# Kernel tuning notes

Hardware: AMD Instinct MI355X
Metric: run time of the kernel (lower is better)

The kernel has to match this reference:

```python
import jax, jax.numpy as jnp
import numpy as np

INPUT_SIZE = 32   # activity vocab
HIDDEN = 512
OUT = 33          # OUT-1 activity logits + 1 duration
COND = 128
LAYERS = 2
MAXLEN = 64
BATCH = 256
SOS = 0
SLOPE = 0.01      # LeakyReLU default negative slope

def _leaky(x):
    return jnp.where(x >= 0, x, SLOPE * x)

def setup_inputs() -> dict:
    key = jax.random.key(0)
    ks = jax.random.split(key, 16)
    s = 0.05  # small init scale keeps gates in a sane range
    return {
        "batch_size": BATCH,
        "h0": jax.random.normal(ks[0], (LAYERS, BATCH, HIDDEN), jnp.float32),
        "c0": jax.random.normal(ks[1], (LAYERS, BATCH, HIDDEN), jnp.float32),
        "conditionals": jax.random.normal(ks[2], (BATCH, COND), jnp.float32),
        "emb": jax.random.normal(ks[3], (INPUT_SIZE, HIDDEN - 1), jnp.float32) * s,
        "Wih": jax.random.normal(ks[4], (LAYERS, 4 * HIDDEN, HIDDEN), jnp.float32) * s,
        "Whh": jax.random.normal(ks[5], (LAYERS, 4 * HIDDEN, HIDDEN), jnp.float32) * s,
        "bih": jax.random.normal(ks[6], (LAYERS, 4 * HIDDEN), jnp.float32) * s,
        "bhh": jax.random.normal(ks[7], (LAYERS, 4 * HIDDEN), jnp.float32) * s,
        "fcW": jax.random.normal(ks[8], (HIDDEN, COND), jnp.float32) * s,
        "fcb": jax.random.normal(ks[9], (HIDDEN,), jnp.float32) * s,
        "fc2W": jax.random.normal(ks[10], (HIDDEN, HIDDEN), jnp.float32) * s,
        "fc2b": jax.random.normal(ks[11], (HIDDEN,), jnp.float32) * s,
        "fc3W": jax.random.normal(ks[12], (OUT, HIDDEN), jnp.float32) * s,
        "fc3b": jax.random.normal(ks[13], (OUT,), jnp.float32) * s,
    }

def reference(batch_size, h0, c0, conditionals, emb, Wih, Whh, bih, bhh,
              fcW, fcb, fc2W, fc2b, fc3W, fc3b):
    B = h0.shape[1]
    # conditionals branch is step-invariant: compute once (same math as per-step fc+LeakyReLU)
    cond = _leaky(conditionals @ fcW.T + fcb)  # [B, H]
    # decoder_input = zeros[B,1,2] with act channel = sos
    inp0 = jnp.concatenate(
        [jnp.full((B, 1), float(SOS), jnp.float32), jnp.zeros((B, 1), jnp.float32)], axis=-1)

    def step(carry, _):
        h, c, inp = carry  # h,c: [L,B,H], inp: [B,2]
        # CustomDurationEmbedding: embed act index, concat duration channel -> [B,H]
        x = jnp.concatenate([emb[inp[:, 0].astype(jnp.int32)], inp[:, 1:]], axis=-1)
        hs, cs = [], []
        for l in range(LAYERS):  # seq_len==1 per step -> one LSTM cell per layer
            g = x @ Wih[l].T + bih[l] + h[l] @ Whh[l].T + bhh[l]  # [B,4H]
            i_g, f_g, g_g, o_g = jnp.split(g, 4, axis=-1)         # torch gate order i,f,g,o
            c_l = jax.nn.sigmoid(f_g) * c[l] + jax.nn.sigmoid(i_g) * jnp.tanh(g_g)
            h_l = jax.nn.sigmoid(o_g) * jnp.tanh(c_l)
            hs.append(h_l); cs.append(c_l)
            x = h_l
        h_new, c_new = jnp.stack(hs), jnp.stack(cs)
        # conditional_add: (lstm_out + cond) -> fc2 -> LeakyReLU -> fc3
        pred = _leaky((x + cond) @ fc2W.T + fc2b) @ fc3W.T + fc3b  # [B,OUT]
        # pack: topk(1) over activity logits; softmax over singleton seq dim == 1.0
        act = jnp.argmax(pred[:, :OUT - 1], axis=-1).astype(pred.dtype)[:, None]
        dur = jnp.ones((B, 1), pred.dtype)
        nxt = jnp.concatenate([act, dur], axis=-1)
        return (h_new, c_new, nxt), pred

    _, outs = jax.lax.scan(step, (h0, c0, inp0), None, length=MAXLEN)  # [T,B,OUT]
    outs = jnp.transpose(outs, (1, 0, 2))  # [B,T,OUT]
    acts_log_probs = jax.nn.log_softmax(outs[..., :OUT - 1], axis=-1)
    durations = jax.nn.softmax(outs[..., OUT - 1:], axis=1)  # Softmax(dim=-2): over time
    return jnp.concatenate([acts_log_probs, durations], axis=-1)
```

## Files before the change

### kernel.cpp

```cpp
#include <hip/hip_runtime.h>
#include <math.h>

#define BB   256
#define HH   512
#define NWG  256
#define NTHR 1024
#define TT   64
#define NOUT 33
#define CD   128
#define SZ   (HH*BB)
#define LOFF (4*HH*HH)
#define BOFF (4*HH)
#define WBLK (16*1024)

typedef float f16v __attribute__((ext_vector_type(16)));
typedef float f8v  __attribute__((ext_vector_type(8)));
typedef const __attribute__((address_space(4))) float  cfloat;
typedef const __attribute__((address_space(4))) f16v   cf16v;
typedef const __attribute__((address_space(4))) f8v    cf8v;

__device__ __forceinline__ float sigm(float x)  { return 1.0f/(1.0f+expf(-x)); }
__device__ __forceinline__ float lrelu(float x) { return x >= 0.0f ? x : 0.01f*x; }

__device__ __forceinline__ float gld(const float* p) {
  return __hip_atomic_load(p, __ATOMIC_RELAXED, __HIP_MEMORY_SCOPE_AGENT);
}
__device__ __forceinline__ void gst(float* p, float v) {
  __hip_atomic_store(p, v, __ATOMIC_RELAXED, __HIP_MEMORY_SCOPE_AGENT);
}

__device__ __forceinline__ cfloat* cptr(const float* p) {
  unsigned long long u = (unsigned long long)p;
  unsigned lo = __builtin_amdgcn_readfirstlane((unsigned)u);
  unsigned hi = __builtin_amdgcn_readfirstlane((unsigned)(u >> 32));
  return (cfloat*)((((unsigned long long)hi) << 32) | (unsigned long long)lo);
}

__device__ __forceinline__ void gbar(unsigned* bar, unsigned ep, int grp, bool fence) {
  __syncthreads();
  if (threadIdx.x == 0) {
    if (fence) __builtin_amdgcn_fence(__ATOMIC_RELEASE, "agent");
    unsigned old = __hip_atomic_fetch_add(&bar[grp*16], 1u, __ATOMIC_RELAXED, __HIP_MEMORY_SCOPE_AGENT);
    if (old == ep*32u + 31u) {
      unsigned o2 = __hip_atomic_fetch_add(&bar[128], 1u, __ATOMIC_RELAXED, __HIP_MEMORY_SCOPE_AGENT);
      if (o2 == ep*8u + 7u)
        __hip_atomic_store(&bar[144], ep+1u, __ATOMIC_RELAXED, __HIP_MEMORY_SCOPE_AGENT);
    }
    while (__hip_atomic_load(&bar[144], __ATOMIC_RELAXED, __HIP_MEMORY_SCOPE_AGENT) < ep+1u)
      __builtin_amdgcn_s_sleep(1);
    if (fence) __builtin_amdgcn_fence(__ATOMIC_ACQUIRE, "agent");
  }
  __syncthreads();
}

extern "C" __global__ void __launch_bounds__(256)
transpose_weights(const float* __restrict__ Wih, const float* __restrict__ Whh,
                  float* __restrict__ wsT)
{
  const int w   = blockIdx.x;
  const int tid = threadIdx.x;
  float* dst = wsT + w*WBLK;
  #pragma unroll 1
  for (int j = 0; j < 64; ++j) {
    int i  = j*256 + tid;
    int ri = i >> 10, k = i & 1023;
    int l  = k >> 9,  kk = k & 511;
    int r2 = ri & 7,  u = r2 >> 2, g = r2 & 3;
    const float* src = (ri < 8) ? Wih : Whh;
    dst[k*16 + ri] = src[l*LOFF + (g*HH + 2*w + u)*HH + kk];
  }
}

__device__ __forceinline__ void FMA2(const f16v& w, float x0, float x1,
                                     float h0, float h1, float* acc) {
  #pragma unroll
  for (int r = 0; r < 8; ++r) {
    acc[r*2+0] += w[r]*x0;
    acc[r*2+1] += w[r]*x1;
  }
  #pragma unroll
  for (int r = 0; r < 8; ++r) {
    acc[r*2+0] += w[8+r]*h0;
    acc[r*2+1] += w[8+r]*h1;
  }
}

__device__ __forceinline__ void lstm_phase(const float* __restrict__ wT,
    const float* __restrict__ bias, float* __restrict__ red,
    const float* __restrict__ xsrc, const float* __restrict__ hsrc,
    float* __restrict__ hdst, float* __restrict__ cbuf,
    int hu0, int tid, int ks, int bg)
{
  const int lane  = tid & 63;
  const int kbase = ks*64;
  const int b0    = bg*128 + lane;
  cf16v* wk = (cf16v*)cptr(wT + kbase*16);
  const float* xp = xsrc + kbase*BB + b0;
  const float* hp = hsrc + kbase*BB + b0;

  float acc[16];
  #pragma unroll
  for (int r = 0; r < 16; ++r) acc[r] = 0.0f;

  float qx[4], qh[4], px[4], ph[4];
  #pragma unroll
  for (int j = 0; j < 2; ++j) {
    qx[j*2] = gld(xp + j*BB); qx[j*2+1] = gld(xp + j*BB + 64);
    qh[j*2] = gld(hp + j*BB); qh[j*2+1] = gld(hp + j*BB + 64);
  }
  #pragma unroll 1
  for (int it = 0; it < 32; ++it) {
    f16v w0 = wk[it*2+0];
    f16v w1 = wk[it*2+1];
    if (it+1 < 32) {
      #pragma unroll
      for (int j = 0; j < 2; ++j) {
        px[j*2]   = gld(xp + (it*2+2+j)*BB);  px[j*2+1] = gld(xp + (it*2+2+j)*BB + 64);
        ph[j*2]   = gld(hp + (it*2+2+j)*BB);  ph[j*2+1] = gld(hp + (it*2+2+j)*BB + 64);
      }
    }
    FMA2(w0, qx[0], qx[1], qh[0], qh[1], acc);
    FMA2(w1, qx[2], qx[3], qh[2], qh[3], acc);
    #pragma unroll
    for (int j = 0; j < 4; ++j) { qx[j] = px[j]; qh[j] = ph[j]; }
  }
  #pragma unroll
  for (int r = 0; r < 8; ++r) {
    red[(ks*8 + r)*BB + b0]      = acc[r*2];
    red[(ks*8 + r)*BB + b0 + 64] = acc[r*2+1];
  }
  __syncthreads();
  if (tid < 512) {
    const int b = tid & 255, u = tid >> 8;
    float g[4];
    #pragma unroll
    for (int gg = 0; gg < 4; ++gg) {
      float s = bias[u*4+gg];
      #pragma unroll
      for (int k2 = 0; k2 < 8; ++k2) s += red[(k2*8 + u*4+gg)*BB + b];
      g[gg] = s;
    }
    const int hu = hu0 + u;
    float ig = sigm(g[0]), fg = sigm(g[1]);
    float gv = tanhf(g[2]), og = sigm(g[3]);
    float cn = fg*cbuf[hu*BB+b] + ig*gv;
    cbuf[hu*BB+b] = cn;
    gst(hdst + hu*BB + b, og*tanhf(cn));
  }
}

extern "C" __global__ void __launch_bounds__(NTHR)
decoder_kernel(const float* __restrict__ h0, const float* __restrict__ c0,
               const float* __restrict__ conds, const float* __restrict__ emb,
               const float* __restrict__ wsT, const float* __restrict__ bih,
               const float* __restrict__ bhh, const float* __restrict__ fcW,
               const float* __restrict__ fcb, const float* __restrict__ fc2W,
               const float* __restrict__ fc2b, const float* __restrict__ fc3W,
               const float* __restrict__ fc3b,
               float* __restrict__ out, unsigned* bar, float* wsf)
{
  const int w   = blockIdx.x;
  const int tid = threadIdx.x;
  const int hu0 = 2*w;
  const int grp = w & 7;
  const int wv  = tid >> 6;
  const int bg  = wv & 1;
  const int ks  = wv >> 1;

  float* xbuf  = wsf;
  float* h1b0  = wsf + 1*SZ;
  float* h1b1  = wsf + 2*SZ;
  float* h2b0  = wsf + 3*SZ;
  float* h2b1  = wsf + 4*SZ;
  float* c1b   = wsf + 5*SZ;
  float* c2b   = wsf + 6*SZ;
  float* condb = wsf + 7*SZ;
  float* yb    = wsf + 8*SZ;
  float* condY = wsf + 9*SZ;

  const float* wT1 = wsT + w*WBLK;
  const float* wT2 = wsT + w*WBLK + 512*16;

  __shared__ float red[64*BB];
  __shared__ float bias1[8], bias2[8], biasc[2];
  __shared__ float lds_y[HH];
  __shared__ float part[NOUT][17];
  __shared__ int   lds_act;
  __shared__ float lds_pad[4096];
  if (tid == 0) ((volatile float*)lds_pad)[0] = 0.0f;

  if (tid < 512) {
    const int b = tid & 255, u = tid >> 8;
    const int k = hu0 + u;
    xbuf[k*BB+b] = (k < HH-1) ? emb[k] : 0.0f;
    h1b0[k*BB+b] = h0[b*HH + k];
    c1b [k*BB+b] = c0[b*HH + k];
    h2b0[k*BB+b] = h0[(BB+b)*HH + k];
    c2b [k*BB+b] = c0[(BB+b)*HH + k];
    float a = fcb[k];
    const float4* cp = (const float4*)(conds + b*CD);
    const float4* wp = (const float4*)(fcW + k*CD);
    #pragma unroll 8
    for (int q = 0; q < CD/4; ++q) {
      float4 c4 = cp[q], w4 = wp[q];
      a += c4.x*w4.x + c4.y*w4.y + c4.z*w4.z + c4.w*w4.w;
    }
    condb[k*BB+b] = lrelu(a);
  }
  if (tid < 8) {
    int u = tid >> 2, g = tid & 3;
    bias1[tid] = bih[g*HH + hu0 + u] + bhh[g*HH + hu0 + u];
    bias2[tid] = bih[BOFF + g*HH + hu0 + u] + bhh[BOFF + g*HH + hu0 + u];
  }
  if (tid < 2) biasc[tid] = fc2b[hu0 + tid];

  unsigned ep = 0;
  gbar(bar, ep++, grp, true);

  if (tid < 512) {
    const int b = tid & 255, u = tid >> 8;
    cfloat* wr = cptr(fc2W + (hu0+u)*HH);
    float s = 0.0f;
    #pragma unroll 4
    for (int k = 0; k < HH; k += 4) {
      s += wr[k]*condb[k*BB+b]     + wr[k+1]*condb[(k+1)*BB+b]
         + wr[k+2]*condb[(k+2)*BB+b] + wr[k+3]*condb[(k+3)*BB+b];
    }
    condY[(hu0+u)*BB + b] = s;
  }
  __syncthreads();

  for (int t = 0; t < TT; ++t) {
    const bool par = (t & 1) != 0;
    float* h1r = par ? h1b1 : h1b0;
    float* h1w = par ? h1b0 : h1b1;
    float* h2r = par ? h2b1 : h2b0;
    float* h2w = par ? h2b0 : h2b1;

    lstm_phase(wT1, bias1, red, xbuf, h1r, h1w, c1b, hu0, tid, ks, bg);
    gbar(bar, ep++, grp, false);
    lstm_phase(wT2, bias2, red, h1w, h2r, h2w, c2b, hu0, tid, ks, bg);
    gbar(bar, ep++, grp, false);
    {
      const int b = tid & 255, s4 = tid >> 8;
      const float* hp = h2w + (s4*128)*BB + b;
      cf8v* w0v = (cf8v*)cptr(fc2W + (hu0+0)*HH + s4*128);
      cf8v* w1v = (cf8v*)cptr(fc2W + (hu0+1)*HH + s4*128);
      float a0 = 0.0f, a1 = 0.0f;
      float q[8], pq[8];
      #pragma unroll
      for (int j = 0; j < 8; ++j) q[j] = gld(hp + j*BB);
      #pragma unroll 1
      for (int it = 0; it < 16; ++it) {
        f8v wa = w0v[it];
        f8v wb = w1v[it];
        if (it+1 < 16) {
          #pragma unroll
          for (int j = 0; j < 8; ++j) pq[j] = gld(hp + (it*8+8+j)*BB);
        }
        #pragma unroll
        for (int j = 0; j < 8; ++j) { a0 += wa[j]*q[j]; a1 += wb[j]*q[j]; }
        #pragma unroll
        for (int j = 0; j < 8; ++j) q[j] = pq[j];
      }
      red[(s4*2+0)*BB + b] = a0;
      red[(s4*2+1)*BB + b] = a1;
    }
    __syncthreads();
    if (tid < 512) {
      const int b = tid & 255, u = tid >> 8;
      float s = biasc[u] + condY[(hu0+u)*BB + b];
      #pragma unroll
      for (int s4 = 0; s4 < 4; ++s4) s += red[(s4*2+u)*BB + b];
      gst(yb + (hu0+u)*BB + b, lrelu(s));
    }
    gbar(bar, ep++, grp, false);
    {
      if (tid < 512) lds_y[tid] = gld(yb + tid*BB + w);
      __syncthreads();
      int o = 0, kc = 0;
      bool active = false;
      if (tid < 512)        { o = tid & 31; kc = tid >> 5; active = true; }
      else if (tid < 528)   { o = 32;       kc = tid - 512; active = true; }
      if (active) {
        float p = 0.0f;
        const float* fw = fc3W + o*HH + kc*32;
        #pragma unroll
        for (int k2 = 0; k2 < 32; ++k2) p += fw[k2] * lds_y[kc*32 + k2];
        part[o][kc] = p;
      }
      __syncthreads();
      float predv = -1e30f;
      if (tid < NOUT) {
        float s = fc3b[tid];
        #pragma unroll
        for (int kc2 = 0; kc2 < 16; ++kc2) s += part[tid][kc2];
        predv = s;
        out[(w*TT + t)*NOUT + tid] = s;
      }
      if (tid < 64) {
        float v  = (tid < 32) ? predv : -1e30f;
        int  idx = tid;
        #pragma unroll
        for (int off = 32; off > 0; off >>= 1) {
          float ov = __shfl_xor(v, off);
          int   oi = __shfl_xor(idx, off);
          if (ov > v || (ov == v && oi < idx)) { v = ov; idx = oi; }
        }
        if (tid == 0) lds_act = idx;
      }
      __syncthreads();
      const int act = lds_act;
      if (tid < 512)
        gst(xbuf + tid*BB + w, (tid < 511) ? emb[act*(HH-1) + tid] : 1.0f);
    }
    gbar(bar, ep++, grp, false);
  }

  if (tid < TT) {
    const int s = tid;
    float* po = out + (w*TT + s)*NOUT;
    float v[NOUT];
    #pragma unroll
    for (int o = 0; o < NOUT; ++o) v[o] = po[o];
    float m = v[0];
    #pragma unroll
    for (int o = 1; o < 32; ++o) m = fmaxf(m, v[o]);
    float sum = 0.0f;
    #pragma unroll
    for (int o = 0; o < 32; ++o) sum += expf(v[o] - m);
    float lse = m + logf(sum);
    #pragma unroll
    for (int o = 0; o < 32; ++o) po[o] = v[o] - lse;
    float d = v[32];
    float dm = d;
    #pragma unroll
    for (int off = 32; off > 0; off >>= 1) dm = fmaxf(dm, __shfl_xor(dm, off));
    float e = expf(d - dm);
    float es = e;
    #pragma unroll
    for (int off = 32; off > 0; off >>= 1) es += __shfl_xor(es, off);
    po[32] = e / es;
  }
}

extern "C" void kernel_launch(void* const* d_in, const int* in_sizes, int n_in,
                              void* d_out, int out_size, void* d_ws, size_t ws_size,
                              hipStream_t stream) {
  const float* h0   = (const float*)d_in[1];
  const float* c0   = (const float*)d_in[2];
  const float* cnd  = (const float*)d_in[3];
  const float* emb  = (const float*)d_in[4];
  const float* Wih  = (const float*)d_in[5];
  const float* Whh  = (const float*)d_in[6];
  const float* bih  = (const float*)d_in[7];
  const float* bhh  = (const float*)d_in[8];
  const float* fcW  = (const float*)d_in[9];
  const float* fcb  = (const float*)d_in[10];
  const float* fc2W = (const float*)d_in[11];
  const float* fc2b = (const float*)d_in[12];
  const float* fc3W = (const float*)d_in[13];
  const float* fc3b = (const float*)d_in[14];

  unsigned* bar = (unsigned*)d_ws;
  float* wsf = (float*)((char*)d_ws + 1024);
  float* wsT = wsf + 10*SZ;

  (void)hipMemsetAsync(d_ws, 0, 1024, stream);

  hipLaunchKernelGGL(transpose_weights, dim3(NWG), dim3(256), 0, stream,
                     Wih, Whh, wsT);
  hipLaunchKernelGGL(decoder_kernel, dim3(NWG), dim3(NTHR), 0, stream,
                     h0, c0, cnd, emb, wsT, bih, bhh, fcW, fcb,
                     fc2W, fc2b, fc3W, fc3b, (float*)d_out, bar, wsf);
}
```

Baseline: 3.731 ms.

## Repartition LSTM work into 4-unit by 128-batch tiles with register cell state

Each workgroup now owns 4 hidden units for half the batch instead of 2 units for the full batch. This halves the per-workgroup weight footprint re-read from the scalar cache relative to the activations and keeps the cell state in registers instead of a global buffer. The fc2 matvec uses a pre-transposed weight block and vectorized float2 activation loads with deeper prefetch. The cost is that each block re-reads the full activation vectors for its half-batch, and the transposed weight layout and barrier schedule change.

```diff
diff --git a/kernel.cpp b/kernel.cpp
--- a/kernel.cpp
+++ b/kernel.cpp
@@ -3,21 +3,18 @@
 
 #define BB   256
 #define HH   512
-#define NWG  256
-#define NTHR 1024
 #define TT   64
 #define NOUT 33
 #define CD   128
+#define NTHR 1024
+#define NWG  256
+#define LOFF (4*HH*HH)
 #define SZ   (HH*BB)
-#define LOFF (4*HH*HH)
-#define BOFF (4*HH)
-#define WBLK (16*1024)
+#define FC2OFF 4194304
 
 typedef float f16v __attribute__((ext_vector_type(16)));
-typedef float f8v  __attribute__((ext_vector_type(8)));
-typedef const __attribute__((address_space(4))) float  cfloat;
-typedef const __attribute__((address_space(4))) f16v   cf16v;
-typedef const __attribute__((address_space(4))) f8v    cf8v;
+typedef const __attribute__((address_space(4))) float cfloat;
+typedef const __attribute__((address_space(4))) f16v  cf16v;
 
 __device__ __forceinline__ float sigm(float x)  { return 1.0f/(1.0f+expf(-x)); }
 __device__ __forceinline__ float lrelu(float x) { return x >= 0.0f ? x : 0.01f*x; }
@@ -25,8 +22,16 @@
 __device__ __forceinline__ float gld(const float* p) {
   return __hip_atomic_load(p, __ATOMIC_RELAXED, __HIP_MEMORY_SCOPE_AGENT);
 }
+__device__ __forceinline__ float2 gld2(const float* p) {
+  unsigned long long v = __hip_atomic_load((const unsigned long long*)p,
+                                           __ATOMIC_RELAXED, __HIP_MEMORY_SCOPE_AGENT);
+  union { unsigned long long u; float2 f; } c; c.u = v; return c.f;
+}
 __device__ __forceinline__ void gst(float* p, float v) {
   __hip_atomic_store(p, v, __ATOMIC_RELAXED, __HIP_MEMORY_SCOPE_AGENT);
+}
+__device__ __forceinline__ unsigned gldu(const unsigned* p) {
+  return __hip_atomic_load(p, __ATOMIC_RELAXED, __HIP_MEMORY_SCOPE_AGENT);
 }
 
 __device__ __forceinline__ cfloat* cptr(const float* p) {
@@ -46,8 +51,7 @@
       if (o2 == ep*8u + 7u)
         __hip_atomic_store(&bar[144], ep+1u, __ATOMIC_RELAXED, __HIP_MEMORY_SCOPE_AGENT);
     }
-    while (__hip_atomic_load(&bar[144], __ATOMIC_RELAXED, __HIP_MEMORY_SCOPE_AGENT) < ep+1u)
-      __builtin_amdgcn_s_sleep(1);
+    while (gldu(&bar[144]) < ep+1u) __builtin_amdgcn_s_sleep(1);
     if (fence) __builtin_amdgcn_fence(__ATOMIC_ACQUIRE, "agent");
   }
   __syncthreads();
@@ -55,236 +59,234 @@
 
 extern "C" __global__ void __launch_bounds__(256)
 transpose_weights(const float* __restrict__ Wih, const float* __restrict__ Whh,
-                  float* __restrict__ wsT)
+                  const float* __restrict__ fc2W, float* __restrict__ wsT)
 {
-  const int w   = blockIdx.x;
-  const int tid = threadIdx.x;
-  float* dst = wsT + w*WBLK;
+  const int i = blockIdx.x, tid = threadIdx.x;
+  float* dst = wsT + (size_t)i*32768;
   #pragma unroll 1
-  for (int j = 0; j < 64; ++j) {
-    int i  = j*256 + tid;
-    int ri = i >> 10, k = i & 1023;
-    int l  = k >> 9,  kk = k & 511;
-    int r2 = ri & 7,  u = r2 >> 2, g = r2 & 3;
-    const float* src = (ri < 8) ? Wih : Whh;
-    dst[k*16 + ri] = src[l*LOFF + (g*HH + 2*w + u)*HH + kk];
-  }
-}
-
-__device__ __forceinline__ void FMA2(const f16v& w, float x0, float x1,
-                                     float h0, float h1, float* acc) {
-  #pragma unroll
-  for (int r = 0; r < 8; ++r) {
-    acc[r*2+0] += w[r]*x0;
-    acc[r*2+1] += w[r]*x1;
-  }
-  #pragma unroll
-  for (int r = 0; r < 8; ++r) {
-    acc[r*2+0] += w[8+r]*h0;
-    acc[r*2+1] += w[8+r]*h1;
-  }
-}
-
-__device__ __forceinline__ void lstm_phase(const float* __restrict__ wT,
+  for (int idx = tid; idx < 32768; idx += 256) {
+    int slot = idx & 15, k = (idx>>4)&511, rh = (idx>>13)&1, l = (idx>>14)&1;
+    int a = slot>>3, r = slot&7, u = r>>2, g = r&3;
+    int hu = i*4 + rh*2 + u;
+    const float* src = a ? Whh : Wih;
+    dst[idx] = src[(size_t)l*LOFF + (size_t)(g*HH+hu)*HH + k];
+  }
+  float* dstf = wsT + FC2OFF + (size_t)i*2048;
+  #pragma unroll 1
+  for (int idx = tid; idx < 2048; idx += 256) {
+    int r = idx & 3, k = idx >> 2;
+    dstf[idx] = fc2W[(size_t)(i*4+r)*HH + k];
+  }
+}
+
+__device__ __forceinline__ void lstm_phase(const float* __restrict__ wTl,
     const float* __restrict__ bias, float* __restrict__ red,
     const float* __restrict__ xsrc, const float* __restrict__ hsrc,
-    float* __restrict__ hdst, float* __restrict__ cbuf,
-    int hu0, int tid, int ks, int bg)
+    float* __restrict__ hdst, float& creg, int i, int j, int tid)
 {
-  const int lane  = tid & 63;
-  const int kbase = ks*64;
-  const int b0    = bg*128 + lane;
-  cf16v* wk = (cf16v*)cptr(wT + kbase*16);
-  const float* xp = xsrc + kbase*BB + b0;
-  const float* hp = hsrc + kbase*BB + b0;
+  const int lane = tid & 63, wvid = tid >> 6;
+  const int rh = wvid & 1, ks = wvid >> 1;
+  cf16v* wp = (cf16v*)cptr(wTl + ((size_t)rh*512 + ks*64)*16);
+  const int bo = j*128 + 2*lane;
+  const float* xp = xsrc + (size_t)(ks*64)*BB + bo;
+  const float* hp = hsrc + (size_t)(ks*64)*BB + bo;
 
   float acc[16];
   #pragma unroll
-  for (int r = 0; r < 16; ++r) acc[r] = 0.0f;
-
-  float qx[4], qh[4], px[4], ph[4];
-  #pragma unroll
-  for (int j = 0; j < 2; ++j) {
-    qx[j*2] = gld(xp + j*BB); qx[j*2+1] = gld(xp + j*BB + 64);
-    qh[j*2] = gld(hp + j*BB); qh[j*2+1] = gld(hp + j*BB + 64);
-  }
+  for (int r = 0; r < 16; ++r) acc[r] = 0.f;
+
+  float2 qx[2], qh[2], px[2], ph[2], rx[2], rhb[2];
+  #pragma unroll
+  for (int kk = 0; kk < 2; ++kk) { qx[kk]=gld2(xp+kk*BB);     qh[kk]=gld2(hp+kk*BB); }
+  #pragma unroll
+  for (int kk = 0; kk < 2; ++kk) { px[kk]=gld2(xp+(2+kk)*BB); ph[kk]=gld2(hp+(2+kk)*BB); }
+
   #pragma unroll 1
-  for (int it = 0; it < 32; ++it) {
-    f16v w0 = wk[it*2+0];
-    f16v w1 = wk[it*2+1];
-    if (it+1 < 32) {
-      #pragma unroll
-      for (int j = 0; j < 2; ++j) {
-        px[j*2]   = gld(xp + (it*2+2+j)*BB);  px[j*2+1] = gld(xp + (it*2+2+j)*BB + 64);
-        ph[j*2]   = gld(hp + (it*2+2+j)*BB);  ph[j*2+1] = gld(hp + (it*2+2+j)*BB + 64);
-      }
-    }
-    FMA2(w0, qx[0], qx[1], qh[0], qh[1], acc);
-    FMA2(w1, qx[2], qx[3], qh[2], qh[3], acc);
-    #pragma unroll
-    for (int j = 0; j < 4; ++j) { qx[j] = px[j]; qh[j] = ph[j]; }
-  }
-  #pragma unroll
-  for (int r = 0; r < 8; ++r) {
-    red[(ks*8 + r)*BB + b0]      = acc[r*2];
-    red[(ks*8 + r)*BB + b0 + 64] = acc[r*2+1];
-  }
+  for (int g = 0; g < 32; ++g) {
+    if (g+2 < 32) {
+      #pragma unroll
+      for (int kk = 0; kk < 2; ++kk) {
+        rx[kk]  = gld2(xp + (g*2+4+kk)*BB);
+        rhb[kk] = gld2(hp + (g*2+4+kk)*BB);
+      }
+    }
+    #pragma unroll
+    for (int kk = 0; kk < 2; ++kk) {
+      f16v w = wp[g*2+kk];
+      float2 xv = qx[kk], hv = qh[kk];
+      #pragma unroll
+      for (int r = 0; r < 8; ++r) {
+        acc[r*2+0] += w[r]*xv.x + w[8+r]*hv.x;
+        acc[r*2+1] += w[r]*xv.y + w[8+r]*hv.y;
+      }
+    }
+    #pragma unroll
+    for (int kk = 0; kk < 2; ++kk) {
+      qx[kk]=px[kk]; qh[kk]=ph[kk]; px[kk]=rx[kk]; ph[kk]=rhb[kk];
+    }
+  }
+  #pragma unroll
+  for (int r = 0; r < 8; ++r)
+    *(float2*)(red + (size_t)(ks*16 + rh*8 + r)*128 + 2*lane) = make_float2(acc[r*2], acc[r*2+1]);
   __syncthreads();
   if (tid < 512) {
-    const int b = tid & 255, u = tid >> 8;
-    float g[4];
+    const int lhu = tid >> 7, b = tid & 127;
+    float g4[4];
     #pragma unroll
     for (int gg = 0; gg < 4; ++gg) {
-      float s = bias[u*4+gg];
-      #pragma unroll
-      for (int k2 = 0; k2 < 8; ++k2) s += red[(k2*8 + u*4+gg)*BB + b];
-      g[gg] = s;
-    }
-    const int hu = hu0 + u;
-    float ig = sigm(g[0]), fg = sigm(g[1]);
-    float gv = tanhf(g[2]), og = sigm(g[3]);
-    float cn = fg*cbuf[hu*BB+b] + ig*gv;
-    cbuf[hu*BB+b] = cn;
-    gst(hdst + hu*BB + b, og*tanhf(cn));
+      float s = bias[lhu*4+gg];
+      #pragma unroll
+      for (int q = 0; q < 8; ++q) s += red[(q*16 + lhu*4+gg)*128 + b];
+      g4[gg] = s;
+    }
+    float ig=sigm(g4[0]), fg=sigm(g4[1]), gv=tanhf(g4[2]), og=sigm(g4[3]);
+    float cn = fg*creg + ig*gv;
+    creg = cn;
+    gst(hdst + (size_t)(i*4+lhu)*BB + j*128 + b, og*tanhf(cn));
+  }
+}
+
+__device__ __forceinline__ void fc2_phase(const float* __restrict__ h2src,
+    const float* __restrict__ wsTf, float* __restrict__ yb,
+    const float* lds_bc, const float* condY_l, float* __restrict__ red,
+    int i, int j, int tid)
+{
+  const int lane = tid & 63, ks2 = tid >> 6;
+  cf16v* wp = (cf16v*)cptr(wsTf + (size_t)ks2*128);
+  const int bo = j*128 + 2*lane;
+  const float* hp = h2src + (size_t)(ks2*32)*BB + bo;
+  float acc[8];
+  #pragma unroll
+  for (int r = 0; r < 8; ++r) acc[r] = 0.f;
+  float2 qh[4], ph[4];
+  #pragma unroll
+  for (int kk = 0; kk < 4; ++kk) qh[kk] = gld2(hp + kk*BB);
+  #pragma unroll 1
+  for (int g = 0; g < 8; ++g) {
+    if (g+1 < 8) {
+      #pragma unroll
+      for (int kk = 0; kk < 4; ++kk) ph[kk] = gld2(hp + (g*4+4+kk)*BB);
+    }
+    f16v w = wp[g];
+    #pragma unroll
+    for (int kk = 0; kk < 4; ++kk) {
+      float2 hv = qh[kk];
+      #pragma unroll
+      for (int r = 0; r < 4; ++r) {
+        acc[r*2+0] += w[kk*4+r]*hv.x;
+        acc[r*2+1] += w[kk*4+r]*hv.y;
+      }
+    }
+    #pragma unroll
+    for (int kk = 0; kk < 4; ++kk) qh[kk] = ph[kk];
+  }
+  #pragma unroll
+  for (int r = 0; r < 4; ++r)
+    *(float2*)(red + (size_t)(ks2*4+r)*128 + 2*lane) = make_float2(acc[r*2], acc[r*2+1]);
+  __syncthreads();
+  if (tid < 512) {
+    int r = tid >> 7, b = tid & 127;
+    float s = lds_bc[r] + condY_l[r*128+b];
+    #pragma unroll
+    for (int q = 0; q < 16; ++q) s += red[(q*4+r)*128 + b];
+    gst(yb + (size_t)(i*4+r)*BB + j*128 + b, lrelu(s));
   }
 }
 
 extern "C" __global__ void __launch_bounds__(NTHR)
 decoder_kernel(const float* __restrict__ h0, const float* __restrict__ c0,
                const float* __restrict__ conds, const float* __restrict__ emb,
-               const float* __restrict__ wsT, const float* __restrict__ bih,
+               const float* __restrict__ wsTW, const float* __restrict__ bih,
                const float* __restrict__ bhh, const float* __restrict__ fcW,
                const float* __restrict__ fcb, const float* __restrict__ fc2W,
                const float* __restrict__ fc2b, const float* __restrict__ fc3W,
                const float* __restrict__ fc3b,
                float* __restrict__ out, unsigned* bar, float* wsf)
 {
-  const int w   = blockIdx.x;
+  const int w = blockIdx.x;
+  const int i = w & 127, j = w >> 7;
+  const int grp = w & 7;
   const int tid = threadIdx.x;
-  const int hu0 = 2*w;
-  const int grp = w & 7;
-  const int wv  = tid >> 6;
-  const int bg  = wv & 1;
-  const int ks  = wv >> 1;
 
   float* xbuf  = wsf;
-  float* h1b0  = wsf + 1*SZ;
-  float* h1b1  = wsf + 2*SZ;
-  float* h2b0  = wsf + 3*SZ;
-  float* h2b1  = wsf + 4*SZ;
-  float* c1b   = wsf + 5*SZ;
-  float* c2b   = wsf + 6*SZ;
-  float* condb = wsf + 7*SZ;
-  float* yb    = wsf + 8*SZ;
-  float* condY = wsf + 9*SZ;
-
-  const float* wT1 = wsT + w*WBLK;
-  const float* wT2 = wsT + w*WBLK + 512*16;
-
-  __shared__ float red[64*BB];
-  __shared__ float bias1[8], bias2[8], biasc[2];
+  float* h1a = wsf + 1*SZ;  float* h1b = wsf + 2*SZ;
+  float* h2a = wsf + 3*SZ;  float* h2b = wsf + 4*SZ;
+  float* yb  = wsf + 5*SZ;
+  float* condb = wsf + 6*SZ;
+  const float* wTi  = wsTW + (size_t)i*32768;
+  const float* wsTf = wsTW + FC2OFF + (size_t)i*2048;
+
+  __shared__ float red[16384];
   __shared__ float lds_y[HH];
   __shared__ float part[NOUT][17];
+  __shared__ float condY_l[512];
+  __shared__ float lds_b1[16], lds_b2[16], lds_bc[4];
   __shared__ int   lds_act;
-  __shared__ float lds_pad[4096];
-  if (tid == 0) ((volatile float*)lds_pad)[0] = 0.0f;
-
+  __shared__ float lds_pad[3072];
+  if (tid == 0) ((volatile float*)lds_pad)[0] = 0.f;
+
+  if (tid < 16) {
+    int u2 = tid >> 2, g = tid & 3;
+    int hu = i*4 + u2;
+    lds_b1[tid] = bih[g*HH+hu] + bhh[g*HH+hu];
+    lds_b2[tid] = bih[4*HH + g*HH+hu] + bhh[4*HH + g*HH+hu];
+  }
+  if (tid < 4) lds_bc[tid] = fc2b[i*4 + tid];
+
+  {
+    int u = tid >> 8, b = tid & 255;
+    int hug = i*4 + u;
+    h1a[(size_t)hug*BB + b] = h0[(size_t)b*HH + hug];
+    h2a[(size_t)hug*BB + b] = h0[(size_t)(BB+b)*HH + hug];
+    xbuf[(size_t)hug*BB + b] = (hug < HH-1) ? emb[hug] : 0.0f;
+    const float* crow = conds + (size_t)b*CD;
+    cfloat* fr = cptr(fcW + (size_t)hug*CD);
+    float s = fcb[hug];
+    #pragma unroll 4
+    for (int q = 0; q < CD; q += 4)
+      s += fr[q]*crow[q] + fr[q+1]*crow[q+1] + fr[q+2]*crow[q+2] + fr[q+3]*crow[q+3];
+    condb[(size_t)hug*BB + b] = lrelu(s);
+  }
+  float c1 = 0.f, c2 = 0.f;
   if (tid < 512) {
-    const int b = tid & 255, u = tid >> 8;
-    const int k = hu0 + u;
-    xbuf[k*BB+b] = (k < HH-1) ? emb[k] : 0.0f;
-    h1b0[k*BB+b] = h0[b*HH + k];
-    c1b [k*BB+b] = c0[b*HH + k];
-    h2b0[k*BB+b] = h0[(BB+b)*HH + k];
-    c2b [k*BB+b] = c0[(BB+b)*HH + k];
-    float a = fcb[k];
-    const float4* cp = (const float4*)(conds + b*CD);
-    const float4* wp = (const float4*)(fcW + k*CD);
-    #pragma unroll 8
-    for (int q = 0; q < CD/4; ++q) {
-      float4 c4 = cp[q], w4 = wp[q];
-      a += c4.x*w4.x + c4.y*w4.y + c4.z*w4.z + c4.w*w4.w;
-    }
-    condb[k*BB+b] = lrelu(a);
-  }
-  if (tid < 8) {
-    int u = tid >> 2, g = tid & 3;
-    bias1[tid] = bih[g*HH + hu0 + u] + bhh[g*HH + hu0 + u];
-    bias2[tid] = bih[BOFF + g*HH + hu0 + u] + bhh[BOFF + g*HH + hu0 + u];
-  }
-  if (tid < 2) biasc[tid] = fc2b[hu0 + tid];
-
+    int lhu = tid >> 7, b = tid & 127;
+    int hug = i*4 + lhu, bg = j*128 + b;
+    c1 = c0[(size_t)bg*HH + hug];
+    c2 = c0[(size_t)(BB+bg)*HH + hug];
+  }
   unsigned ep = 0;
   gbar(bar, ep++, grp, true);
 
   if (tid < 512) {
-    const int b = tid & 255, u = tid >> 8;
-    cfloat* wr = cptr(fc2W + (hu0+u)*HH);
-    float s = 0.0f;
+    int r = tid >> 7, b = tid & 127, bg = j*128 + b;
+    cfloat* wr = cptr(fc2W + (size_t)(i*4+r)*HH);
+    float s = 0.f;
     #pragma unroll 4
-    for (int k = 0; k < HH; k += 4) {
-      s += wr[k]*condb[k*BB+b]     + wr[k+1]*condb[(k+1)*BB+b]
-         + wr[k+2]*condb[(k+2)*BB+b] + wr[k+3]*condb[(k+3)*BB+b];
-    }
-    condY[(hu0+u)*BB + b] = s;
+    for (int k = 0; k < HH; ++k) s += wr[k]*condb[(size_t)k*BB + bg];
+    condY_l[r*128 + b] = s;
   }
   __syncthreads();
 
   for (int t = 0; t < TT; ++t) {
-    const bool par = (t & 1) != 0;
-    float* h1r = par ? h1b1 : h1b0;
-    float* h1w = par ? h1b0 : h1b1;
-    float* h2r = par ? h2b1 : h2b0;
-    float* h2w = par ? h2b0 : h2b1;
-
-    lstm_phase(wT1, bias1, red, xbuf, h1r, h1w, c1b, hu0, tid, ks, bg);
+    float* h1r = (t&1) ? h1b : h1a;  float* h1w = (t&1) ? h1a : h1b;
+    float* h2r = (t&1) ? h2b : h2a;  float* h2w = (t&1) ? h2a : h2b;
+
+    lstm_phase(wTi,         lds_b1, red, xbuf, h1r, h1w, c1, i, j, tid);
     gbar(bar, ep++, grp, false);
-    lstm_phase(wT2, bias2, red, h1w, h2r, h2w, c2b, hu0, tid, ks, bg);
+    lstm_phase(wTi + 16384, lds_b2, red, h1w, h2r, h2w, c2, i, j, tid);
+    gbar(bar, ep++, grp, false);
+    fc2_phase(h2w, wsTf, yb, lds_bc, condY_l, red, i, j, tid);
     gbar(bar, ep++, grp, false);
     {
-      const int b = tid & 255, s4 = tid >> 8;
-      const float* hp = h2w + (s4*128)*BB + b;
-      cf8v* w0v = (cf8v*)cptr(fc2W + (hu0+0)*HH + s4*128);
-      cf8v* w1v = (cf8v*)cptr(fc2W + (hu0+1)*HH + s4*128);
-      float a0 = 0.0f, a1 = 0.0f;
-      float q[8], pq[8];
-      #pragma unroll
-      for (int j = 0; j < 8; ++j) q[j] = gld(hp + j*BB);
-      #pragma unroll 1
-      for (int it = 0; it < 16; ++it) {
-        f8v wa = w0v[it];
-        f8v wb = w1v[it];
-        if (it+1 < 16) {
-          #pragma unroll
-          for (int j = 0; j < 8; ++j) pq[j] = gld(hp + (it*8+8+j)*BB);
-        }
-        #pragma unroll
-        for (int j = 0; j < 8; ++j) { a0 += wa[j]*q[j]; a1 += wb[j]*q[j]; }
-        #pragma unroll
-        for (int j = 0; j < 8; ++j) q[j] = pq[j];
-      }
-      red[(s4*2+0)*BB + b] = a0;
-      red[(s4*2+1)*BB + b] = a1;
-    }
-    __syncthreads();
-    if (tid < 512) {
-      const int b = tid & 255, u = tid >> 8;
-      float s = biasc[u] + condY[(hu0+u)*BB + b];
-      #pragma unroll
-      for (int s4 = 0; s4 < 4; ++s4) s += red[(s4*2+u)*BB + b];
-      gst(yb + (hu0+u)*BB + b, lrelu(s));
-    }
-    gbar(bar, ep++, grp, false);
-    {
-      if (tid < 512) lds_y[tid] = gld(yb + tid*BB + w);
+      if (tid < 512) lds_y[tid] = gld(yb + (size_t)tid*BB + w);
       __syncthreads();
       int o = 0, kc = 0;
       bool active = false;
-      if (tid < 512)        { o = tid & 31; kc = tid >> 5; active = true; }
-      else if (tid < 528)   { o = 32;       kc = tid - 512; active = true; }
+      if (tid < 512)      { o = tid & 31; kc = tid >> 5; active = true; }
+      else if (tid < 528) { o = 32;       kc = tid - 512; active = true; }
       if (active) {
-        float p = 0.0f;
-        const float* fw = fc3W + o*HH + kc*32;
+        float p = 0.f;
+        const float* fw = fc3W + (size_t)o*HH + kc*32;
         #pragma unroll
         for (int k2 = 0; k2 < 32; ++k2) p += fw[k2] * lds_y[kc*32 + k2];
         part[o][kc] = p;
@@ -296,7 +298,7 @@
         #pragma unroll
         for (int kc2 = 0; kc2 < 16; ++kc2) s += part[tid][kc2];
         predv = s;
-        out[(w*TT + t)*NOUT + tid] = s;
+        out[(size_t)(w*TT + t)*NOUT + tid] = s;
       }
       if (tid < 64) {
         float v  = (tid < 32) ? predv : -1e30f;
@@ -312,21 +314,21 @@
       __syncthreads();
       const int act = lds_act;
       if (tid < 512)
-        gst(xbuf + tid*BB + w, (tid < 511) ? emb[act*(HH-1) + tid] : 1.0f);
+        gst(xbuf + (size_t)tid*BB + w, (tid < HH-1) ? emb[(size_t)act*(HH-1) + tid] : 1.0f);
     }
     gbar(bar, ep++, grp, false);
   }
 
   if (tid < TT) {
     const int s = tid;
-    float* po = out + (w*TT + s)*NOUT;
+    float* po = out + (size_t)(w*TT + s)*NOUT;
     float v[NOUT];
     #pragma unroll
     for (int o = 0; o < NOUT; ++o) v[o] = po[o];
     float m = v[0];
     #pragma unroll
     for (int o = 1; o < 32; ++o) m = fmaxf(m, v[o]);
-    float sum = 0.0f;
+    float sum = 0.f;
     #pragma unroll
     for (int o = 0; o < 32; ++o) sum += expf(v[o] - m);
     float lse = m + logf(sum);
@@ -364,12 +366,12 @@
 
   unsigned* bar = (unsigned*)d_ws;
   float* wsf = (float*)((char*)d_ws + 1024);
-  float* wsT = wsf + 10*SZ;
+  float* wsT = wsf + 7*SZ;
 
   (void)hipMemsetAsync(d_ws, 0, 1024, stream);
 
-  hipLaunchKernelGGL(transpose_weights, dim3(NWG), dim3(256), 0, stream,
-                     Wih, Whh, wsT);
+  hipLaunchKernelGGL(transpose_weights, dim3(128), dim3(256), 0, stream,
+                     Wih, Whh, fc2W, wsT);
   hipLaunchKernelGGL(decoder_kernel, dim3(NWG), dim3(NTHR), 0, stream,
                      h0, c0, cnd, emb, wsT, bih, bhh, fcW, fcb,
                      fc2W, fc2b, fc3W, fc3b, (float*)d_out, bar, wsf);
```

Result: slower. 4.567 ms (+22.4%).
